# Kernel optimization log

Measured on AMD Instinct MI355X. Metric: run time of the kernel, lower is better.

The kernel has to match this reference:

```python
import jax, jax.numpy as jnp
import numpy as np

B, N, FEAT, HID = 1024, 128, 512, 256


def setup_inputs() -> dict:
    key = jax.random.key(0)
    k1, k2, k3, k4, k5, k6 = jax.random.split(key, 6)
    x = jax.random.normal(k1, (B, FEAT), dtype=jnp.float32)
    labels = jax.random.randint(k2, (B,), 0, N, dtype=jnp.int64)
    W_proj = jax.random.normal(k3, (FEAT, HID), dtype=jnp.float32) / np.sqrt(FEAT)
    b_proj = jax.random.normal(k4, (HID,), dtype=jnp.float32) * 0.01
    means = jax.random.normal(k5, (N, HID), dtype=jnp.float32)
    # inverse covariances must be SPD so sqrt(dist_sq) is real
    A = jax.random.normal(k6, (N, HID, HID), dtype=jnp.float32)
    inv_covs = jnp.einsum('nij,nkj->nik', A, A) / HID + 0.1 * jnp.eye(HID, dtype=jnp.float32)
    return {"x": x, "labels": labels, "W_proj": W_proj, "b_proj": b_proj,
            "means": means, "inv_covs": inv_covs}


def reference(x, labels, W_proj, b_proj, means, inv_covs):
    b = x.shape[0]
    n = means.shape[0]
    x_proj = x @ W_proj + b_proj                       # (b, hid)
    delta = x_proj[:, None, :] - means[None, :, :]     # (b, n, hid)
    # batched Mahalanobis quadratic form
    dist_sq = jnp.einsum('bni,nij,bnj->bn', delta, inv_covs, delta)
    distmat = jnp.sqrt(dist_sq + 1e-12)                # (b, n)
    center_mask = (labels[:, None] == jnp.arange(n)[None, :]).astype(distmat.dtype)
    loss = jnp.clip(distmat * center_mask, 1e-12, 1e12).sum() / b
    return loss, distmat
```

## Files before the change

kernel.cpp:

```cpp
#include <hip/hip_runtime.h>
#include <hip/hip_bf16.h>

#define B_    1024
#define N_    128
#define FEAT_ 512
#define HID_  256

typedef __bf16 bf16x8 __attribute__((ext_vector_type(8)));
typedef float  f32x4  __attribute__((ext_vector_type(4)));

__device__ __forceinline__ unsigned int f2bf(float f) {
    unsigned int u = __float_as_uint(f);
    u += 0x7fffu + ((u >> 16) & 1u);
    return u >> 16;
}
__device__ __forceinline__ unsigned int pack2(float a, float b) {
    return f2bf(a) | (f2bf(b) << 16);
}

__global__ __launch_bounds__(256) void prep_kernel(
    const float* __restrict__ x, const float* __restrict__ W,
    const float* __restrict__ bias, const float* __restrict__ means,
    const float* __restrict__ invcov,
    float* __restrict__ pproj, unsigned short* __restrict__ Mbf,
    float* __restrict__ v2, float* __restrict__ cpart, float* __restrict__ out)
{
    const int t = threadIdx.x;
    if (blockIdx.x < 1024) {
        if (blockIdx.x == 0 && t == 0) out[0] = (float)(N_ - 1) * 1e-12f;
        const int c   = blockIdx.x & 3;
        const int g   = blockIdx.x >> 2;
        const int r   = t & 3;
        const int h0  = (t >> 2) * 4;
        const int row = g * 4 + r;
        const float* xr = x + (size_t)row * FEAT_ + c * 128;
        const float* Wc = W + (size_t)c * 128 * HID_;
        float4 acc = make_float4(0.f, 0.f, 0.f, 0.f);
        if (c == 0) acc = *(const float4*)(bias + h0);
        #pragma unroll 4
        for (int f = 0; f < 128; f += 4) {
            const float4 xv = *(const float4*)(xr + f);
            const float4 w0 = *(const float4*)(Wc + (size_t)(f + 0) * HID_ + h0);
            const float4 w1 = *(const float4*)(Wc + (size_t)(f + 1) * HID_ + h0);
            const float4 w2 = *(const float4*)(Wc + (size_t)(f + 2) * HID_ + h0);
            const float4 w3 = *(const float4*)(Wc + (size_t)(f + 3) * HID_ + h0);
            acc.x += xv.x * w0.x + xv.y * w1.x + xv.z * w2.x + xv.w * w3.x;
            acc.y += xv.x * w0.y + xv.y * w1.y + xv.z * w2.y + xv.w * w3.y;
            acc.z += xv.x * w0.z + xv.y * w1.z + xv.z * w2.z + xv.w * w3.z;
            acc.w += xv.x * w0.w + xv.y * w1.w + xv.z * w2.w + xv.w * w3.w;
        }
        *(float4*)(pproj + (size_t)c * (B_ * HID_) + (size_t)row * HID_ + h0) = acc;
    } else {
        __shared__ float sv[16][33];
        __shared__ float sw[2];
        const int cb = blockIdx.x - 1024;
        const int n  = cb >> 4;
        const int jg = cb & 15;
        const float* Mn = invcov + (size_t)n * (HID_ * HID_) + (size_t)jg * 16 * HID_;
        const float* mu = means + (size_t)n * HID_;
        unsigned short* Mb = Mbf + (size_t)n * (HID_ * HID_) + (size_t)jg * 16 * HID_;
        const int gc = t & 31;
        const int r0 = t >> 5;
        const float* s0 = Mn + (size_t)r0 * HID_ + gc * 8;
        const float* s1 = Mn + (size_t)(r0 + 8) * HID_ + gc * 8;
        const float4 a0 = *(const float4*)s0;
        const float4 b0 = *(const float4*)(s0 + 4);
        const float4 a1 = *(const float4*)s1;
        const float4 b1 = *(const float4*)(s1 + 4);
        const float4 mk0 = *(const float4*)(mu + gc * 8);
        const float4 mk1 = *(const float4*)(mu + gc * 8 + 4);
        const int g20 = gc ^ ((r0 & 7) << 2);
        const int g21 = gc ^ (((r0 + 8) & 7) << 2);
        *(uint4*)(Mb + (size_t)r0 * HID_ + g20 * 8) =
            make_uint4(pack2(a0.x, a0.y), pack2(a0.z, a0.w), pack2(b0.x, b0.y), pack2(b0.z, b0.w));
        *(uint4*)(Mb + (size_t)(r0 + 8) * HID_ + g21 * 8) =
            make_uint4(pack2(a1.x, a1.y), pack2(a1.z, a1.w), pack2(b1.x, b1.y), pack2(b1.z, b1.w));
        sv[r0][gc]     = a0.x * mk0.x + a0.y * mk0.y + a0.z * mk0.z + a0.w * mk0.w
                       + b0.x * mk1.x + b0.y * mk1.y + b0.z * mk1.z + b0.w * mk1.w;
        sv[r0 + 8][gc] = a1.x * mk0.x + a1.y * mk0.y + a1.z * mk0.z + a1.w * mk0.w
                       + b1.x * mk1.x + b1.y * mk1.y + b1.z * mk1.z + b1.w * mk1.w;
        __syncthreads();
        if (t < 128) {
            const int row = t >> 3;
            const int i0  = (t & 7) * 4;
            float v = sv[row][i0] + sv[row][i0 + 1] + sv[row][i0 + 2] + sv[row][i0 + 3];
            v += __shfl_xor(v, 1);
            v += __shfl_xor(v, 2);
            v += __shfl_xor(v, 4);
            const int j = jg * 16 + row;
            if ((t & 7) == 0) v2[(size_t)n * HID_ + j] = 2.f * v;
            float cc = ((t & 7) == 0) ? v * mu[j] : 0.f;
            cc += __shfl_xor(cc, 8);
            cc += __shfl_xor(cc, 16);
            cc += __shfl_xor(cc, 32);
            if ((t & 63) == 0) sw[t >> 6] = cc;
        }
        __syncthreads();
        if (t == 0) cpart[cb] = sw[0] + sw[1];
    }
}

__global__ __launch_bounds__(256) void projsum_kernel(
    const float* __restrict__ pproj, float* __restrict__ xp,
    unsigned short* __restrict__ xbf)
{
    const int i = blockIdx.x * 256 + threadIdx.x;
    const float4 a = ((const float4*)pproj)[i];
    const float4 b = ((const float4*)pproj)[i +  65536];
    const float4 c = ((const float4*)pproj)[i + 131072];
    const float4 d = ((const float4*)pproj)[i + 196608];
    float4 s;
    s.x = (a.x + b.x) + (c.x + d.x);
    s.y = (a.y + b.y) + (c.y + d.y);
    s.z = (a.z + b.z) + (c.z + d.z);
    s.w = (a.w + b.w) + (c.w + d.w);
    ((float4*)xp)[i] = s;
    ((uint2*)xbf)[i] = make_uint2(pack2(s.x, s.y), pack2(s.z, s.w));
}

__global__ __launch_bounds__(512, 4) void dist_kernel(
    const float* __restrict__ xp, const unsigned short* __restrict__ xbf,
    const unsigned short* __restrict__ Mbf, const float* __restrict__ v2,
    float* __restrict__ p)
{
    extern __shared__ unsigned short Ms[];

    const int tid  = threadIdx.x;
    const int bh   = blockIdx.x;
    const int jh   = blockIdx.y;
    const int n    = blockIdx.z;
    const int wave = tid >> 6;
    const int lane = tid & 63;
    const int q    = lane >> 4;
    const int l    = lane & 15;

    const unsigned short* src = Mbf + (size_t)n * (HID_ * HID_) + (size_t)jh * 32768;
    #pragma unroll
    for (int i = 0; i < 8; ++i) {
        const int c = i * 8 + wave;
        __builtin_amdgcn_global_load_lds(
            (const __attribute__((address_space(1))) unsigned int*)(src + (size_t)c * 512 + lane * 8),
            (__attribute__((address_space(3))) unsigned int*)&Ms[c * 512],
            16, 0, 0);
    }

    bf16x8 afrag[2][8];
    #pragma unroll
    for (int rb = 0; rb < 2; ++rb) {
        const unsigned short* xr = xbf + (size_t)(bh * 256 + wave * 32 + rb * 16 + l) * HID_;
        #pragma unroll
        for (int kk = 0; kk < 8; ++kk)
            afrag[rb][kk] = *(const bf16x8*)(xr + kk * 32 + q * 8);
    }
    float v2l[8];
    #pragma unroll
    for (int ct = 0; ct < 8; ++ct)
        v2l[ct] = v2[(size_t)n * HID_ + jh * 128 + ct * 16 + l];

    __syncthreads();

    float part[8];
    #pragma unroll
    for (int i = 0; i < 8; ++i) part[i] = 0.f;

    const size_t xbase = (size_t)(bh * 256 + wave * 32 + q * 4) * HID_ + jh * 128 + l;

    #pragma unroll
    for (int ct = 0; ct < 8; ++ct) {
        float xl[8];
        #pragma unroll
        for (int rb = 0; rb < 2; ++rb)
            #pragma unroll
            for (int r = 0; r < 4; ++r)
                xl[rb * 4 + r] = xp[xbase + (size_t)(rb * 16 + r) * HID_ + ct * 16];

        f32x4 acc0 = {0.f,0.f,0.f,0.f}, acc1 = {0.f,0.f,0.f,0.f};
        #pragma unroll
        for (int kk = 0; kk < 8; ++kk) {
            const bf16x8 bfrag = *(const bf16x8*)&Ms[(ct * 16 + l) * HID_ +
                                                     (((kk * 4 + q) ^ ((l & 7) << 2)) << 3)];
            acc0 = __builtin_amdgcn_mfma_f32_16x16x32_bf16(afrag[0][kk], bfrag, acc0, 0, 0, 0);
            acc1 = __builtin_amdgcn_mfma_f32_16x16x32_bf16(afrag[1][kk], bfrag, acc1, 0, 0, 0);
        }
        const float vv = v2l[ct];
        #pragma unroll
        for (int r = 0; r < 4; ++r) {
            part[r]     += (acc0[r] - vv) * xl[r];
            part[4 + r] += (acc1[r] - vv) * xl[4 + r];
        }
    }

    #pragma unroll
    for (int i = 0; i < 8; ++i) {
        float v = part[i];
        v += __shfl_xor(v, 1);
        v += __shfl_xor(v, 2);
        v += __shfl_xor(v, 4);
        v += __shfl_xor(v, 8);
        part[i] = v;
    }
    if (l == 0) {
        float* pb = p + (size_t)jh * (B_ * N_);
        #pragma unroll
        for (int i = 0; i < 8; ++i) {
            const int row = bh * 256 + wave * 32 + (i >> 2) * 16 + q * 4 + (i & 3);
            pb[(size_t)row * N_ + n] = part[i];
        }
    }
}

__global__ __launch_bounds__(256) void finalize_kernel(
    const float* __restrict__ p, const float* __restrict__ cpart,
    const int* __restrict__ labels, float* __restrict__ out)
{
    __shared__ float sc[128];
    const int t = threadIdx.x;
    if (t < 128) {
        float s = 0.f;
        #pragma unroll
        for (int g = 0; g < 16; ++g) s += cpart[t * 16 + g];
        sc[t] = s;
    }
    __syncthreads();
    const int i = blockIdx.x * 256 + t;
    const int n = i & (N_ - 1);
    const int b = i >> 7;
    const float d = sqrtf(p[i] + p[B_ * N_ + i] + sc[n] + 1e-12f);
    out[1 + i] = d;
    float c = (labels[b] == n) ? d * (1.f / (float)B_) : 0.f;
    c += __shfl_xor(c, 1);
    c += __shfl_xor(c, 2);
    c += __shfl_xor(c, 4);
    c += __shfl_xor(c, 8);
    c += __shfl_xor(c, 16);
    c += __shfl_xor(c, 32);
    if ((t & 63) == 0 && c != 0.f) atomicAdd(out, c);
}

extern "C" void kernel_launch(void* const* d_in, const int* in_sizes, int n_in,
                              void* d_out, int out_size, void* d_ws, size_t ws_size,
                              hipStream_t stream) {
    const float* x      = (const float*)d_in[0];
    const int*   labels = (const int*)d_in[1];
    const float* W      = (const float*)d_in[2];
    const float* bias   = (const float*)d_in[3];
    const float* means  = (const float*)d_in[4];
    const float* invcov = (const float*)d_in[5];
    float* out = (float*)d_out;

    char* ws = (char*)d_ws;
    unsigned short* Mbf   = (unsigned short*)(ws);
    float*          xp    = (float*)         (ws + 16777216);
    unsigned short* xbf   = (unsigned short*)(ws + 17825792);
    float*          v2    = (float*)         (ws + 18350080);
    float*          cpart = (float*)         (ws + 18481152);
    float*          p     = (float*)         (ws + 18489344);
    float*          pproj = (float*)         (ws + 19537920);

    constexpr int DIST_LDS = 128 * HID_ * 2;
    (void)hipFuncSetAttribute((const void*)dist_kernel,
                              hipFuncAttributeMaxDynamicSharedMemorySize, DIST_LDS);

    prep_kernel<<<dim3(3072), 256, 0, stream>>>(x, W, bias, means, invcov,
                                                pproj, Mbf, v2, cpart, out);
    projsum_kernel<<<dim3(256), 256, 0, stream>>>(pproj, xp, xbf);
    dist_kernel<<<dim3(4, 2, N_), 512, DIST_LDS, stream>>>(xp, xbf, Mbf, v2, p);
    finalize_kernel<<<dim3((B_ * N_) / 256), 256, 0, stream>>>(p, cpart, labels, out);
}
```

Before: 162.4 us.

## Fuse finalize into dist kernel with double-buffered LDS over full hidden dim

The dist kernel now gives each block the whole hidden dimension instead of splitting it in two. The split-j grid dimension goes away, and the block streams the 256 rows of M through a double-buffered 64-row LDS ring with async global-to-LDS loads. Because each block now holds the complete quadratic form, it computes sqrt, writes distmat, and accumulates the masked loss directly. This removes the partial-sum buffer round trip and the separate finalize launch. In exchange the grid has half as many blocks, and each block does more serial work with a barrier per stage.

```diff
diff --git a/kernel.cpp b/kernel.cpp
--- a/kernel.cpp
+++ b/kernel.cpp
@@ -121,23 +121,24 @@
 __global__ __launch_bounds__(512, 4) void dist_kernel(
     const float* __restrict__ xp, const unsigned short* __restrict__ xbf,
     const unsigned short* __restrict__ Mbf, const float* __restrict__ v2,
-    float* __restrict__ p)
+    const float* __restrict__ cpart, const int* __restrict__ labels,
+    float* __restrict__ out)
 {
     extern __shared__ unsigned short Ms[];
 
     const int tid  = threadIdx.x;
     const int bh   = blockIdx.x;
-    const int jh   = blockIdx.y;
-    const int n    = blockIdx.z;
+    const int n    = blockIdx.y;
     const int wave = tid >> 6;
     const int lane = tid & 63;
     const int q    = lane >> 4;
     const int l    = lane & 15;
 
-    const unsigned short* src = Mbf + (size_t)n * (HID_ * HID_) + (size_t)jh * 32768;
-    #pragma unroll
-    for (int i = 0; i < 8; ++i) {
-        const int c = i * 8 + wave;
+    const unsigned short* src = Mbf + (size_t)n * (HID_ * HID_);
+
+    #pragma unroll
+    for (int i = 0; i < 4; ++i) {
+        const int c = wave * 4 + i;
         __builtin_amdgcn_global_load_lds(
             (const __attribute__((address_space(1))) unsigned int*)(src + (size_t)c * 512 + lane * 8),
             (__attribute__((address_space(3))) unsigned int*)&Ms[c * 512],
@@ -152,10 +153,9 @@
         for (int kk = 0; kk < 8; ++kk)
             afrag[rb][kk] = *(const bf16x8*)(xr + kk * 32 + q * 8);
     }
-    float v2l[8];
-    #pragma unroll
-    for (int ct = 0; ct < 8; ++ct)
-        v2l[ct] = v2[(size_t)n * HID_ + jh * 128 + ct * 16 + l];
+    float cn = 0.f;
+    #pragma unroll
+    for (int g = 0; g < 16; ++g) cn += cpart[n * 16 + g];
 
     __syncthreads();
 
@@ -163,31 +163,49 @@
     #pragma unroll
     for (int i = 0; i < 8; ++i) part[i] = 0.f;
 
-    const size_t xbase = (size_t)(bh * 256 + wave * 32 + q * 4) * HID_ + jh * 128 + l;
-
-    #pragma unroll
-    for (int ct = 0; ct < 8; ++ct) {
-        float xl[8];
+    const size_t xbase = (size_t)(bh * 256 + wave * 32 + q * 4) * HID_ + l;
+
+    #pragma unroll
+    for (int p = 0; p < 4; ++p) {
+        if (p < 3) {
+            const unsigned short* sq = src + (size_t)(p + 1) * 16384;
+            unsigned short* dq = &Ms[((p + 1) & 1) * 16384];
+            #pragma unroll
+            for (int i = 0; i < 4; ++i) {
+                const int c = wave * 4 + i;
+                __builtin_amdgcn_global_load_lds(
+                    (const __attribute__((address_space(1))) unsigned int*)(sq + (size_t)c * 512 + lane * 8),
+                    (__attribute__((address_space(3))) unsigned int*)(dq + c * 512),
+                    16, 0, 0);
+            }
+        }
+        const unsigned short* buf = &Ms[(p & 1) * 16384];
         #pragma unroll
-        for (int rb = 0; rb < 2; ++rb)
-            #pragma unroll
-            for (int r = 0; r < 4; ++r)
-                xl[rb * 4 + r] = xp[xbase + (size_t)(rb * 16 + r) * HID_ + ct * 16];
-
-        f32x4 acc0 = {0.f,0.f,0.f,0.f}, acc1 = {0.f,0.f,0.f,0.f};
-        #pragma unroll
-        for (int kk = 0; kk < 8; ++kk) {
-            const bf16x8 bfrag = *(const bf16x8*)&Ms[(ct * 16 + l) * HID_ +
-                                                     (((kk * 4 + q) ^ ((l & 7) << 2)) << 3)];
-            acc0 = __builtin_amdgcn_mfma_f32_16x16x32_bf16(afrag[0][kk], bfrag, acc0, 0, 0, 0);
-            acc1 = __builtin_amdgcn_mfma_f32_16x16x32_bf16(afrag[1][kk], bfrag, acc1, 0, 0, 0);
-        }
-        const float vv = v2l[ct];
-        #pragma unroll
-        for (int r = 0; r < 4; ++r) {
-            part[r]     += (acc0[r] - vv) * xl[r];
-            part[4 + r] += (acc1[r] - vv) * xl[4 + r];
-        }
+        for (int ct2 = 0; ct2 < 4; ++ct2) {
+            const int ct = p * 4 + ct2;
+            const float vv = v2[(size_t)n * HID_ + ct * 16 + l];
+            float xl[8];
+            #pragma unroll
+            for (int rb = 0; rb < 2; ++rb)
+                #pragma unroll
+                for (int r = 0; r < 4; ++r)
+                    xl[rb * 4 + r] = xp[xbase + (size_t)(rb * 16 + r) * HID_ + ct * 16];
+
+            f32x4 acc0 = {0.f,0.f,0.f,0.f}, acc1 = {0.f,0.f,0.f,0.f};
+            #pragma unroll
+            for (int kk = 0; kk < 8; ++kk) {
+                const bf16x8 bfrag = *(const bf16x8*)&buf[(ct2 * 16 + l) * HID_ +
+                                                          (((kk * 4 + q) ^ ((l & 7) << 2)) << 3)];
+                acc0 = __builtin_amdgcn_mfma_f32_16x16x32_bf16(afrag[0][kk], bfrag, acc0, 0, 0, 0);
+                acc1 = __builtin_amdgcn_mfma_f32_16x16x32_bf16(afrag[1][kk], bfrag, acc1, 0, 0, 0);
+            }
+            #pragma unroll
+            for (int r = 0; r < 4; ++r) {
+                part[r]     += (acc0[r] - vv) * xl[r];
+                part[4 + r] += (acc1[r] - vv) * xl[4 + r];
+            }
+        }
+        __syncthreads();
     }
 
     #pragma unroll
@@ -199,42 +217,19 @@
         v += __shfl_xor(v, 8);
         part[i] = v;
     }
+    float c = 0.f;
     if (l == 0) {
-        float* pb = p + (size_t)jh * (B_ * N_);
         #pragma unroll
         for (int i = 0; i < 8; ++i) {
             const int row = bh * 256 + wave * 32 + (i >> 2) * 16 + q * 4 + (i & 3);
-            pb[(size_t)row * N_ + n] = part[i];
-        }
-    }
-}
-
-__global__ __launch_bounds__(256) void finalize_kernel(
-    const float* __restrict__ p, const float* __restrict__ cpart,
-    const int* __restrict__ labels, float* __restrict__ out)
-{
-    __shared__ float sc[128];
-    const int t = threadIdx.x;
-    if (t < 128) {
-        float s = 0.f;
-        #pragma unroll
-        for (int g = 0; g < 16; ++g) s += cpart[t * 16 + g];
-        sc[t] = s;
-    }
-    __syncthreads();
-    const int i = blockIdx.x * 256 + t;
-    const int n = i & (N_ - 1);
-    const int b = i >> 7;
-    const float d = sqrtf(p[i] + p[B_ * N_ + i] + sc[n] + 1e-12f);
-    out[1 + i] = d;
-    float c = (labels[b] == n) ? d * (1.f / (float)B_) : 0.f;
-    c += __shfl_xor(c, 1);
-    c += __shfl_xor(c, 2);
-    c += __shfl_xor(c, 4);
-    c += __shfl_xor(c, 8);
+            const float d = sqrtf(part[i] + cn + 1e-12f);
+            out[1 + (size_t)row * N_ + n] = d;
+            if (labels[row] == n) c += d;
+        }
+    }
     c += __shfl_xor(c, 16);
     c += __shfl_xor(c, 32);
-    if ((t & 63) == 0 && c != 0.f) atomicAdd(out, c);
+    if (lane == 0 && c != 0.f) atomicAdd(out, c * (1.f / (float)B_));
 }
 
 extern "C" void kernel_launch(void* const* d_in, const int* in_sizes, int n_in,
@@ -254,16 +249,15 @@
     unsigned short* xbf   = (unsigned short*)(ws + 17825792);
     float*          v2    = (float*)         (ws + 18350080);
     float*          cpart = (float*)         (ws + 18481152);
-    float*          p     = (float*)         (ws + 18489344);
-    float*          pproj = (float*)         (ws + 19537920);
-
-    constexpr int DIST_LDS = 128 * HID_ * 2;
+    float*          pproj = (float*)         (ws + 18489344);
+
+    constexpr int DIST_LDS = 2 * 64 * HID_ * 2;
     (void)hipFuncSetAttribute((const void*)dist_kernel,
                               hipFuncAttributeMaxDynamicSharedMemorySize, DIST_LDS);
 
     prep_kernel<<<dim3(3072), 256, 0, stream>>>(x, W, bias, means, invcov,
                                                 pproj, Mbf, v2, cpart, out);
     projsum_kernel<<<dim3(256), 256, 0, stream>>>(pproj, xp, xbf);
-    dist_kernel<<<dim3(4, 2, N_), 512, DIST_LDS, stream>>>(xp, xbf, Mbf, v2, p);
-    finalize_kernel<<<dim3((B_ * N_) / 256), 256, 0, stream>>>(p, cpart, labels, out);
-}
+    dist_kernel<<<dim3(4, N_), 512, DIST_LDS, stream>>>(xp, xbf, Mbf, v2, cpart,
+                                                        labels, out);
+}
```

Measured after the change: 175.3 us. +7.9%, slower.
